# Kernel optimization log

Measured on AMD Instinct MI355X. Metric: run time of the kernel, lower is better.

The kernel has to match this reference:

```python
import jax, jax.numpy as jnp
import numpy as np

B, L, C, H, W = 4, 4096, 1024, 16, 512
D = C // H            # head_dim = 64
STRIDE = W // 2


def setup_inputs() -> dict:
    key = jax.random.key(0)
    k0, k1, k2 = jax.random.split(key, 3)
    s = 0.02
    return {
        "x": jax.random.normal(k0, (B, L, C), jnp.float32),
        "w_qkv": jax.random.normal(k1, (C, 3 * C), jnp.float32) * s,
        "b_qkv": jnp.zeros((3 * C,), jnp.float32),
        "w_out": jax.random.normal(k2, (C, C), jnp.float32) * s,
        "b_out": jnp.zeros((C,), jnp.float32),
    }


def _local_attention(x, w_qkv, b_qkv, w_out, b_out):
    b, l, c = x.shape
    pad = (-l) % W  # pad seq to multiple of window_size (0 here)
    x = jnp.pad(x, ((0, 0), (0, pad), (0, 0)))
    lp = l + pad
    qkv = (x @ w_qkv + b_qkv).reshape(b, lp, 3, H, D).transpose(2, 0, 3, 1, 4)
    q, k, v = qkv[0], qkv[1], qkv[2]  # each [B, H, Lp, D]
    nw = (lp - W) // STRIDE + 1       # number of overlapping windows
    # window token indices [nw, W]
    idx = jnp.arange(nw)[:, None] * STRIDE + jnp.arange(W)[None, :]
    qw = q[:, :, idx, :]  # [B, H, nw, W, D]
    kw = k[:, :, idx, :]
    vw = v[:, :, idx, :]
    # non-causal (bidirectional=True) attention within each window,
    # flash-attn default softmax scale = head_dim**-0.5
    scores = jnp.einsum('bhnqd,bhnkd->bhnqk', qw, kw) / jnp.sqrt(jnp.float32(D))
    probs = jax.nn.softmax(scores, axis=-1)
    ow = jnp.einsum('bhnqk,bhnkd->bhnqd', probs, vw)  # [B, H, nw, W, D]
    # concatenate window outputs along sequence, back to [B, nw*W, C]
    o = ow.transpose(0, 2, 3, 1, 4).reshape(b, nw * W, c)
    o = o @ w_out + b_out
    return o[:, :l, :]


def reference(x, w_qkv, b_qkv, w_out, b_out):
    return _local_attention(x, w_qkv, b_qkv, w_out, b_out)
```

## Files before the change

kernel.cpp:

```cpp
#include <hip/hip_runtime.h>

#define LQ 2304

typedef __attribute__((ext_vector_type(8))) short bf16x8;
typedef __attribute__((ext_vector_type(8))) unsigned short u16x8;
typedef __attribute__((ext_vector_type(4))) float f32x4;
typedef __attribute__((ext_vector_type(4))) unsigned int u32x4;

#define MFMA(a, b, c) __builtin_amdgcn_mfma_f32_16x16x32_bf16((a), (b), (c), 0, 0, 0)
#define AS1 __attribute__((address_space(1)))
#define AS3 __attribute__((address_space(3)))

static __device__ __forceinline__ unsigned short f2bf(float f) {
  unsigned int u = __builtin_bit_cast(unsigned int, f);
  u += 0x7fffu + ((u >> 16) & 1u);
  return (unsigned short)(u >> 16);
}

static __device__ __forceinline__ unsigned int pkbf(float hi, float lo) {
  return __builtin_amdgcn_perm(__builtin_bit_cast(unsigned int, hi),
                               __builtin_bit_cast(unsigned int, lo), 0x07060302u);
}

static __device__ __forceinline__ void lds16(const unsigned short* g, unsigned short* l) {
  __builtin_amdgcn_global_load_lds((AS1 const unsigned int*)g, (AS3 unsigned int*)l, 16, 0, 0);
}

static __device__ __forceinline__ void transpose_body(const float* __restrict__ src,
                                                      unsigned short* __restrict__ dst,
                                                      int K, int N, int bx, int by, int tid,
                                                      float (*t)[33]) {
  int bn = bx * 32, bk = by * 32;
  int tx = tid & 31, ty = tid >> 5;
  for (int i = ty; i < 32; i += 8)
    t[i][tx] = src[(size_t)(bk + i) * N + bn + tx];
  __syncthreads();
  for (int i = ty; i < 32; i += 8)
    dst[(size_t)(bn + i) * K + bk + tx] = f2bf(t[tx][i]);
}

__global__ __launch_bounds__(256) void preprocess(const float* __restrict__ x,
                                                  unsigned short* __restrict__ xbf,
                                                  const float* __restrict__ wqkv,
                                                  unsigned short* __restrict__ wqkvT,
                                                  const float* __restrict__ wout,
                                                  unsigned short* __restrict__ woutT) {
  __shared__ float t[32][33];
  int bid = blockIdx.x, tid = threadIdx.x;
  if (bid < 4608) {
    int idx = bid * 256 + tid;
    int b = idx / 294912;
    int g = idx - b * 294912;
    int row = g >> 7, c8 = (g & 127) * 8;
    const float* src = x + ((size_t)b * 4096 + row) * 1024 + c8;
    float4 f0 = *(const float4*)src;
    float4 f1 = *(const float4*)(src + 4);
    u16x8 u;
    u[0] = f2bf(f0.x); u[1] = f2bf(f0.y); u[2] = f2bf(f0.z); u[3] = f2bf(f0.w);
    u[4] = f2bf(f1.x); u[5] = f2bf(f1.y); u[6] = f2bf(f1.z); u[7] = f2bf(f1.w);
    *(u16x8*)(xbf + ((size_t)b * 2304 + row) * 1024 + c8) = u;
  } else if (bid < 7680) {
    int tb = bid - 4608;
    transpose_body(wqkv, wqkvT, 1024, 3072, tb % 96, tb / 96, tid, t);
  } else {
    int tb = bid - 7680;
    transpose_body(wout, woutT, 1024, 1024, tb & 31, tb >> 5, tid, t);
  }
}

#define K2SCALE 0.18033688011112042f
__global__ __launch_bounds__(256) void qkv_gemm(const unsigned short* __restrict__ xbf,
                                                const float* __restrict__ bqkv,
                                                const unsigned short* __restrict__ wT,
                                                unsigned short* __restrict__ qws,
                                                unsigned short* __restrict__ kws,
                                                unsigned short* __restrict__ vws) {
  __shared__ __align__(16) unsigned short As[128 * 64];
  __shared__ __align__(16) unsigned short Bs[128 * 64];
  const int tid = threadIdx.x;
  const int mt = blockIdx.y;
  const int nt = blockIdx.x;
  const int bidx = mt / 18;
  const int l0 = (mt % 18) * 128;
  const int n0 = nt * 128;
  const int lane = tid & 63, wv = tid >> 6;
  const int wm = (wv >> 1) * 64, wn = (wv & 1) * 64;
  const int l16 = lane & 15, quad = lane >> 4;

  const int srow = lane >> 3;
  const int sc = ((lane & 7) ^ srow) * 8;
  const unsigned short* ga = xbf + ((size_t)(bidx * LQ + l0 + wv * 32 + srow)) * 1024 + sc;
  const unsigned short* gb = wT + ((size_t)(n0 + wv * 32 + srow)) * 1024 + sc;
  unsigned short* la = As + wv * 2048;
  unsigned short* lb = Bs + wv * 2048;
  const int xsw = (l16 & 7) * 8;

  const f32x4 zero4 = {0.f, 0.f, 0.f, 0.f};
  f32x4 acc[4][4];
#pragma unroll
  for (int i = 0; i < 4; i++)
#pragma unroll
    for (int j = 0; j < 4; j++) acc[i][j] = zero4;

  for (int k0 = 0; k0 < 1024; k0 += 64) {
    __syncthreads();
#pragma unroll
    for (int j = 0; j < 4; j++) {
      lds16(ga + j * 8 * 1024, la + j * 512);
      lds16(gb + j * 8 * 1024, lb + j * 512);
    }
    __syncthreads();
#pragma unroll
    for (int h = 0; h < 2; h++) {
      bf16x8 af[4], bfv[4];
#pragma unroll
      for (int i = 0; i < 4; i++)
        af[i] = *(const bf16x8*)(&As[(wm + i * 16 + l16) * 64 + (((h << 5) + quad * 8) ^ xsw)]);
#pragma unroll
      for (int j = 0; j < 4; j++)
        bfv[j] = *(const bf16x8*)(&Bs[(wn + j * 16 + l16) * 64 + (((h << 5) + quad * 8) ^ xsw)]);
#pragma unroll
      for (int i = 0; i < 4; i++)
#pragma unroll
        for (int j = 0; j < 4; j++)
          acc[i][j] = MFMA(af[i], bfv[j], acc[i][j]);
    }
    ga += 64;
    gb += 64;
  }

#pragma unroll
  for (int j = 0; j < 4; j++) {
    int col = n0 + wn + j * 16 + l16;
    int which = col >> 10;
    int hcol = (col >> 6) & 15;
    int dcol = col & 63;
    unsigned short* dst = which == 0 ? qws : (which == 1 ? kws : vws);
    float scale = which == 0 ? K2SCALE : 1.0f;
    float bias = bqkv[col];
    size_t cbase = ((size_t)bidx * 16 + hcol) * LQ * 64 + dcol;
#pragma unroll
    for (int i = 0; i < 4; i++) {
      int lrow = l0 + wm + i * 16 + quad * 4;
#pragma unroll
      for (int r = 0; r < 4; r++)
        dst[cbase + (size_t)(lrow + r) * 64] = f2bf((acc[i][j][r] + bias) * scale);
    }
  }
}

#define KSTR 72
#define VSTRT 136

__global__ __launch_bounds__(512, 2) void attn_kernel(const unsigned short* __restrict__ q,
                                                      const unsigned short* __restrict__ k,
                                                      const unsigned short* __restrict__ v,
                                                      unsigned short* __restrict__ o) {
  __shared__ __align__(16) unsigned short Ks[128 * KSTR];
  __shared__ __align__(16) unsigned short Vt[64 * VSTRT];
  const int n = blockIdx.x, h = blockIdx.y, b = blockIdx.z;
  const size_t base = (((size_t)b * 16 + h) * LQ + n * 256) * 64;
  const unsigned short* qg = q + base;
  const unsigned short* kg = k + base;
  const unsigned short* vg = v + base;
  const int tid = threadIdx.x;
  const int lane = tid & 63, wv = tid >> 6;
  const int l16 = lane & 15, quad = lane >> 4;
  const f32x4 zero4 = {0.f, 0.f, 0.f, 0.f};
  const float RB = 0.002815015607053277f;

  bf16x8 qf0[4], qf1[4];
#pragma unroll
  for (int qs = 0; qs < 4; qs++) {
    int qrow = wv * 64 + qs * 16 + l16;
    qf0[qs] = *(const bf16x8*)(qg + (size_t)qrow * 64 + quad * 8);
    qf1[qs] = *(const bf16x8*)(qg + (size_t)qrow * 64 + quad * 8 + 32);
  }
  f32x4 O[4][4];
#pragma unroll
  for (int qs = 0; qs < 4; qs++)
#pragma unroll
    for (int dt = 0; dt < 4; dt++) O[qs][dt] = zero4;
  float lsum[4] = {0.f, 0.f, 0.f, 0.f};

  for (int kt = 0; kt < 4; kt++) {
    __syncthreads();
#pragma unroll
    for (int it = 0; it < 2; it++) {
      int i = it * 512 + tid;
      int key = i >> 3, part = i & 7;
      *(u16x8*)(&Ks[key * KSTR + part * 8]) =
          *(const u16x8*)(kg + (size_t)(kt * 128 + key) * 64 + part * 8);
    }
#pragma unroll
    for (int it = 0; it < 2; it++) {
      int key = it * 64 + lane;
      u16x8 raw = *(const u16x8*)(vg + (size_t)(kt * 128 + key) * 64 + wv * 8);
      int pos = (key & ~31) + ((key >> 2) & 3) * 8 + ((key >> 4) & 1) * 4 + (key & 3);
#pragma unroll
      for (int t = 0; t < 8; t++) Vt[(wv * 8 + t) * VSTRT + pos] = raw[t];
    }
    __syncthreads();

    for (int c = 0; c < 4; c++) {
      const unsigned short* kr0 = &Ks[(c * 32 + l16) * KSTR + quad * 8];
      bf16x8 ka0 = *(const bf16x8*)kr0;
      bf16x8 ka1 = *(const bf16x8*)(kr0 + 32);
      bf16x8 kb0 = *(const bf16x8*)(kr0 + 16 * KSTR);
      bf16x8 kb1 = *(const bf16x8*)(kr0 + 16 * KSTR + 32);
      bf16x8 vf[4];
#pragma unroll
      for (int dt = 0; dt < 4; dt++)
        vf[dt] = *(const bf16x8*)(&Vt[(dt * 16 + l16) * VSTRT + c * 32 + quad * 8]);
#pragma unroll
      for (int qs = 0; qs < 4; qs++) {
        f32x4 s0 = zero4, s1 = zero4;
        s0 = MFMA(ka0, qf0[qs], s0);
        s0 = MFMA(ka1, qf1[qs], s0);
        s1 = MFMA(kb0, qf0[qs], s1);
        s1 = MFMA(kb1, qf1[qs], s1);
        float p0[4], p1[4], ls = 0.f;
#pragma unroll
        for (int r = 0; r < 4; r++) {
          p0[r] = __builtin_amdgcn_exp2f(s0[r] + RB);
          p1[r] = __builtin_amdgcn_exp2f(s1[r] + RB);
          ls += p0[r] + p1[r];
        }
        lsum[qs] += ls;
        u32x4 pw;
        pw[0] = pkbf(p0[1], p0[0]);
        pw[1] = pkbf(p0[3], p0[2]);
        pw[2] = pkbf(p1[1], p1[0]);
        pw[3] = pkbf(p1[3], p1[2]);
        bf16x8 pf = __builtin_bit_cast(bf16x8, pw);
#pragma unroll
        for (int dt = 0; dt < 4; dt++)
          O[qs][dt] = MFMA(pf, vf[dt], O[qs][dt]);
      }
    }
  }

#pragma unroll
  for (int qs = 0; qs < 4; qs++) {
    float ls = lsum[qs];
    ls += __shfl_xor(ls, 16);
    ls += __shfl_xor(ls, 32);
    float linv = 1.0f / ls;
    float li[4];
#pragma unroll
    for (int r = 0; r < 4; r++) li[r] = __shfl(linv, quad * 4 + r);
    size_t orow = (size_t)b * 4096 + n * 512 + wv * 64 + qs * 16;
#pragma unroll
    for (int dt = 0; dt < 4; dt++) {
      int col = h * 64 + dt * 16 + l16;
#pragma unroll
      for (int r = 0; r < 4; r++)
        o[(orow + quad * 4 + r) * 1024 + col] = f2bf(O[qs][dt][r] * li[r]);
    }
  }
}

__global__ __launch_bounds__(256) void out_gemm(const unsigned short* __restrict__ A,
                                                const unsigned short* __restrict__ wT,
                                                const float* __restrict__ bout,
                                                float* __restrict__ out) {
  __shared__ __align__(16) unsigned short As[128 * 64];
  __shared__ __align__(16) unsigned short Bs[128 * 64];
  const int tid = threadIdx.x;
  const int m0 = blockIdx.y * 128;
  const int n0 = blockIdx.x * 128;
  const int lane = tid & 63, wv = tid >> 6;
  const int wm = (wv >> 1) * 64, wn = (wv & 1) * 64;
  const int l16 = lane & 15, quad = lane >> 4;

  const int srow = lane >> 3;
  const int sc = ((lane & 7) ^ srow) * 8;
  const unsigned short* ga = A + ((size_t)(m0 + wv * 32 + srow)) * 1024 + sc;
  const unsigned short* gb = wT + ((size_t)(n0 + wv * 32 + srow)) * 1024 + sc;
  unsigned short* la = As + wv * 2048;
  unsigned short* lb = Bs + wv * 2048;
  const int xsw = (l16 & 7) * 8;

  const f32x4 zero4 = {0.f, 0.f, 0.f, 0.f};
  f32x4 acc[4][4];
#pragma unroll
  for (int i = 0; i < 4; i++)
#pragma unroll
    for (int j = 0; j < 4; j++) acc[i][j] = zero4;

  for (int k0 = 0; k0 < 1024; k0 += 64) {
    __syncthreads();
#pragma unroll
    for (int j = 0; j < 4; j++) {
      lds16(ga + j * 8 * 1024, la + j * 512);
      lds16(gb + j * 8 * 1024, lb + j * 512);
    }
    __syncthreads();
#pragma unroll
    for (int h = 0; h < 2; h++) {
      bf16x8 af[4], bfv[4];
#pragma unroll
      for (int i = 0; i < 4; i++)
        af[i] = *(const bf16x8*)(&As[(wm + i * 16 + l16) * 64 + (((h << 5) + quad * 8) ^ xsw)]);
#pragma unroll
      for (int j = 0; j < 4; j++)
        bfv[j] = *(const bf16x8*)(&Bs[(wn + j * 16 + l16) * 64 + (((h << 5) + quad * 8) ^ xsw)]);
#pragma unroll
      for (int i = 0; i < 4; i++)
#pragma unroll
        for (int j = 0; j < 4; j++)
          acc[i][j] = MFMA(af[i], bfv[j], acc[i][j]);
    }
    ga += 64;
    gb += 64;
  }

#pragma unroll
  for (int j = 0; j < 4; j++) {
    int col = n0 + wn + j * 16 + l16;
    float bias = bout[col];
#pragma unroll
    for (int i = 0; i < 4; i++) {
      int row = m0 + wm + i * 16 + quad * 4;
#pragma unroll
      for (int r = 0; r < 4; r++)
        out[(size_t)(row + r) * 1024 + col] = acc[i][j][r] + bias;
    }
  }
}

#define WQKVT_OFF 0u
#define WOUTT_OFF (WQKVT_OFF + 3072u * 1024u * 2u)
#define QWS_OFF   (WOUTT_OFF + 1024u * 1024u * 2u)
#define KVQ_SZ    (4u * 16u * 2304u * 64u * 2u)
#define KWS_OFF   (QWS_OFF + KVQ_SZ)
#define VWS_OFF   (KWS_OFF + KVQ_SZ)
#define OWS_OFF   (VWS_OFF + KVQ_SZ)
#define XBF_OFF   OWS_OFF

extern "C" void kernel_launch(void* const* d_in, const int* in_sizes, int n_in,
                              void* d_out, int out_size, void* d_ws, size_t ws_size,
                              hipStream_t stream) {
  const float* x     = (const float*)d_in[0];
  const float* w_qkv = (const float*)d_in[1];
  const float* b_qkv = (const float*)d_in[2];
  const float* w_out = (const float*)d_in[3];
  const float* b_out = (const float*)d_in[4];
  float* out = (float*)d_out;
  char* ws = (char*)d_ws;

  unsigned short* wqkvT = (unsigned short*)(ws + WQKVT_OFF);
  unsigned short* woutT = (unsigned short*)(ws + WOUTT_OFF);
  unsigned short* qws   = (unsigned short*)(ws + QWS_OFF);
  unsigned short* kws   = (unsigned short*)(ws + KWS_OFF);
  unsigned short* vws   = (unsigned short*)(ws + VWS_OFF);
  unsigned short* ows   = (unsigned short*)(ws + OWS_OFF);
  unsigned short* xbf   = (unsigned short*)(ws + XBF_OFF);

  preprocess<<<8704, 256, 0, stream>>>(x, xbf, w_qkv, wqkvT, w_out, woutT);

  qkv_gemm<<<dim3(24, 72), 256, 0, stream>>>(xbf, b_qkv, wqkvT, qws, kws, vws);

  attn_kernel<<<dim3(8, 16, 4), 512, 0, stream>>>(qws, kws, vws, ows);

  out_gemm<<<dim3(8, 128), 256, 0, stream>>>(ows, woutT, b_out, out);
}
```

Measured before the change: 330.8 us.

## Pre-transpose V in QKV GEMM, double-buffer K/V via async LDS loads

The QKV GEMM epilogue now writes V in a transposed, pre-permuted layout so the attention kernel no longer does a scalar transpose into shared memory. The attention kernel double-buffers K and V tiles with direct global-to-LDS loads using XOR swizzles, overlapping the next tile's load with the current tile's MFMAs. It also adds s_setprio around MFMA groups, stages the output through LDS for coalesced 16-byte stores, and reorders the grid so heads and batches vary fastest. In exchange it uses more LDS per block, which may limit occupancy, and the V epilogue stores become strided along the sequence dimension.

```diff
diff --git a/kernel.cpp b/kernel.cpp
--- a/kernel.cpp
+++ b/kernel.cpp
@@ -4,6 +4,7 @@
 
 typedef __attribute__((ext_vector_type(8))) short bf16x8;
 typedef __attribute__((ext_vector_type(8))) unsigned short u16x8;
+typedef __attribute__((ext_vector_type(4))) unsigned short u16x4;
 typedef __attribute__((ext_vector_type(4))) float f32x4;
 typedef __attribute__((ext_vector_type(4))) unsigned int u32x4;
 
@@ -135,39 +136,66 @@
     int which = col >> 10;
     int hcol = (col >> 6) & 15;
     int dcol = col & 63;
-    unsigned short* dst = which == 0 ? qws : (which == 1 ? kws : vws);
-    float scale = which == 0 ? K2SCALE : 1.0f;
     float bias = bqkv[col];
-    size_t cbase = ((size_t)bidx * 16 + hcol) * LQ * 64 + dcol;
-#pragma unroll
-    for (int i = 0; i < 4; i++) {
-      int lrow = l0 + wm + i * 16 + quad * 4;
-#pragma unroll
-      for (int r = 0; r < 4; r++)
-        dst[cbase + (size_t)(lrow + r) * 64] = f2bf((acc[i][j][r] + bias) * scale);
-    }
-  }
-}
-
-#define KSTR 72
-#define VSTRT 136
+    if (which == 2) {
+      size_t vbase = (((size_t)bidx * 16 + hcol) * 64 + dcol) * (size_t)LQ;
+#pragma unroll
+      for (int i = 0; i < 4; i++) {
+        int lrow = l0 + wm + i * 16 + quad * 4;
+        int pbase = (lrow & ~31) | (((lrow >> 2) & 3) << 3) | (((lrow >> 4) & 1) << 2);
+        u16x4 st;
+#pragma unroll
+        for (int r = 0; r < 4; r++) st[r] = f2bf(acc[i][j][r] + bias);
+        *(u16x4*)(vws + vbase + pbase) = st;
+      }
+    } else {
+      unsigned short* dst = which == 0 ? qws : kws;
+      float scale = which == 0 ? K2SCALE : 1.0f;
+      size_t cbase = ((size_t)bidx * 16 + hcol) * ((size_t)LQ * 64) + dcol;
+#pragma unroll
+      for (int i = 0; i < 4; i++) {
+        int lrow = l0 + wm + i * 16 + quad * 4;
+#pragma unroll
+        for (int r = 0; r < 4; r++)
+          dst[cbase + (size_t)(lrow + r) * 64] = f2bf((acc[i][j][r] + bias) * scale);
+      }
+    }
+  }
+}
 
 __global__ __launch_bounds__(512, 2) void attn_kernel(const unsigned short* __restrict__ q,
                                                       const unsigned short* __restrict__ k,
-                                                      const unsigned short* __restrict__ v,
+                                                      const unsigned short* __restrict__ vT,
                                                       unsigned short* __restrict__ o) {
-  __shared__ __align__(16) unsigned short Ks[128 * KSTR];
-  __shared__ __align__(16) unsigned short Vt[64 * VSTRT];
-  const int n = blockIdx.x, h = blockIdx.y, b = blockIdx.z;
+  __shared__ __align__(16) unsigned short Ks[2 * 8192];
+  __shared__ __align__(16) unsigned short Vt[2 * 8192];
+  const int hb = blockIdx.x, n = blockIdx.y;
+  const int h = hb & 15, b = hb >> 4;
   const size_t base = (((size_t)b * 16 + h) * LQ + n * 256) * 64;
   const unsigned short* qg = q + base;
   const unsigned short* kg = k + base;
-  const unsigned short* vg = v + base;
+  const unsigned short* vg = vT + ((size_t)b * 16 + h) * 64 * (size_t)LQ + n * 256;
   const int tid = threadIdx.x;
   const int lane = tid & 63, wv = tid >> 6;
   const int l16 = lane & 15, quad = lane >> 4;
+  const int h7 = l16 & 7;
   const f32x4 zero4 = {0.f, 0.f, 0.f, 0.f};
   const float RB = 0.002815015607053277f;
+
+  const int skey = tid >> 3;
+  const unsigned short* ks0 = kg + (size_t)skey * 64 + (((tid & 7) ^ (skey & 7)) * 8);
+  const int sd = tid >> 4;
+  const unsigned short* vs0 = vg + (size_t)sd * LQ + (((tid & 15) ^ (sd & 7)) * 8);
+  unsigned short* kl = Ks + wv * 512;
+  unsigned short* vl = Vt + wv * 512;
+
+#define STAGE(t, sel)                                          \
+  do {                                                         \
+    lds16(ks0 + (t) * 8192, kl + (sel) * 8192);                \
+    lds16(ks0 + (t) * 8192 + 4096, kl + (sel) * 8192 + 4096);  \
+    lds16(vs0 + (t) * 128, vl + (sel) * 8192);                 \
+    lds16(vs0 + (t) * 128 + (size_t)32 * LQ, vl + (sel) * 8192 + 4096); \
+  } while (0)
 
   bf16x8 qf0[4], qf1[4];
 #pragma unroll
@@ -183,42 +211,34 @@
     for (int dt = 0; dt < 4; dt++) O[qs][dt] = zero4;
   float lsum[4] = {0.f, 0.f, 0.f, 0.f};
 
+  STAGE(0, 0);
+  __syncthreads();
+
+#pragma unroll
   for (int kt = 0; kt < 4; kt++) {
-    __syncthreads();
-#pragma unroll
-    for (int it = 0; it < 2; it++) {
-      int i = it * 512 + tid;
-      int key = i >> 3, part = i & 7;
-      *(u16x8*)(&Ks[key * KSTR + part * 8]) =
-          *(const u16x8*)(kg + (size_t)(kt * 128 + key) * 64 + part * 8);
-    }
-#pragma unroll
-    for (int it = 0; it < 2; it++) {
-      int key = it * 64 + lane;
-      u16x8 raw = *(const u16x8*)(vg + (size_t)(kt * 128 + key) * 64 + wv * 8);
-      int pos = (key & ~31) + ((key >> 2) & 3) * 8 + ((key >> 4) & 1) * 4 + (key & 3);
-#pragma unroll
-      for (int t = 0; t < 8; t++) Vt[(wv * 8 + t) * VSTRT + pos] = raw[t];
-    }
-    __syncthreads();
-
+    const int sel = kt & 1;
+    if (kt < 3) STAGE(kt + 1, sel ^ 1);
+    const unsigned short* Kb = Ks + sel * 8192;
+    const unsigned short* Vb = Vt + sel * 8192;
     for (int c = 0; c < 4; c++) {
-      const unsigned short* kr0 = &Ks[(c * 32 + l16) * KSTR + quad * 8];
-      bf16x8 ka0 = *(const bf16x8*)kr0;
-      bf16x8 ka1 = *(const bf16x8*)(kr0 + 32);
-      bf16x8 kb0 = *(const bf16x8*)(kr0 + 16 * KSTR);
-      bf16x8 kb1 = *(const bf16x8*)(kr0 + 16 * KSTR + 32);
+      const int ra = (c * 32 + l16) * 64;
+      bf16x8 ka0 = *(const bf16x8*)(Kb + ra + ((quad ^ h7) * 8));
+      bf16x8 ka1 = *(const bf16x8*)(Kb + ra + (((quad + 4) ^ h7) * 8));
+      bf16x8 kb0 = *(const bf16x8*)(Kb + ra + 1024 + ((quad ^ h7) * 8));
+      bf16x8 kb1 = *(const bf16x8*)(Kb + ra + 1024 + (((quad + 4) ^ h7) * 8));
       bf16x8 vf[4];
 #pragma unroll
       for (int dt = 0; dt < 4; dt++)
-        vf[dt] = *(const bf16x8*)(&Vt[(dt * 16 + l16) * VSTRT + c * 32 + quad * 8]);
+        vf[dt] = *(const bf16x8*)(Vb + (dt * 16 + l16) * 128 + (((c * 4 + quad) ^ h7) * 8));
 #pragma unroll
       for (int qs = 0; qs < 4; qs++) {
         f32x4 s0 = zero4, s1 = zero4;
+        __builtin_amdgcn_s_setprio(1);
         s0 = MFMA(ka0, qf0[qs], s0);
         s0 = MFMA(ka1, qf1[qs], s0);
         s1 = MFMA(kb0, qf0[qs], s1);
         s1 = MFMA(kb1, qf1[qs], s1);
+        __builtin_amdgcn_s_setprio(0);
         float p0[4], p1[4], ls = 0.f;
 #pragma unroll
         for (int r = 0; r < 4; r++) {
@@ -233,13 +253,18 @@
         pw[2] = pkbf(p1[1], p1[0]);
         pw[3] = pkbf(p1[3], p1[2]);
         bf16x8 pf = __builtin_bit_cast(bf16x8, pw);
+        __builtin_amdgcn_s_setprio(1);
 #pragma unroll
         for (int dt = 0; dt < 4; dt++)
           O[qs][dt] = MFMA(pf, vf[dt], O[qs][dt]);
+        __builtin_amdgcn_s_setprio(0);
       }
     }
-  }
-
+    __syncthreads();
+  }
+#undef STAGE
+
+  unsigned short* ow = (wv < 4) ? (Ks + wv * 4096) : (Vt + (wv - 4) * 4096);
 #pragma unroll
   for (int qs = 0; qs < 4; qs++) {
     float ls = lsum[qs];
@@ -249,14 +274,20 @@
     float li[4];
 #pragma unroll
     for (int r = 0; r < 4; r++) li[r] = __shfl(linv, quad * 4 + r);
-    size_t orow = (size_t)b * 4096 + n * 512 + wv * 64 + qs * 16;
-#pragma unroll
-    for (int dt = 0; dt < 4; dt++) {
-      int col = h * 64 + dt * 16 + l16;
+#pragma unroll
+    for (int dt = 0; dt < 4; dt++)
 #pragma unroll
       for (int r = 0; r < 4; r++)
-        o[(orow + quad * 4 + r) * 1024 + col] = f2bf(O[qs][dt][r] * li[r]);
-    }
+        ow[(qs * 16 + quad * 4 + r) * 64 + dt * 16 + l16] = f2bf(O[qs][dt][r] * li[r]);
+  }
+  __syncthreads();
+  const size_t orow0 = (size_t)b * 4096 + n * 512 + wv * 64;
+  const int rrow = lane >> 3, rch = lane & 7;
+#pragma unroll
+  for (int i = 0; i < 8; i++) {
+    int row = i * 8 + rrow;
+    u16x8 val = *(const u16x8*)(ow + row * 64 + rch * 8);
+    *(u16x8*)(o + (orow0 + row) * 1024 + h * 64 + rch * 8) = val;
   }
 }
 
@@ -361,7 +392,7 @@
 
   qkv_gemm<<<dim3(24, 72), 256, 0, stream>>>(xbf, b_qkv, wqkvT, qws, kws, vws);
 
-  attn_kernel<<<dim3(8, 16, 4), 512, 0, stream>>>(qws, kws, vws, ows);
+  attn_kernel<<<dim3(64, 8, 1), 512, 0, stream>>>(qws, kws, vws, ows);
 
   out_gemm<<<dim3(8, 128), 256, 0, stream>>>(ows, woutT, b_out, out);
 }
```

Measured after the change: 508.7 us. 53.8% more time.
